# Performance work log

Hardware: AMD Instinct MI355X
Metric: run time of the kernel (lower is better)

## Reference

```python
import jax, jax.numpy as jnp
import numpy as np

B, T, V, E, U, D1, D2, C = 256, 512, 32000, 100, 512, 1024, 1024, 10
SCALE = 0.02


def setup_inputs() -> dict:
    key = jax.random.key(0)
    ks = jax.random.split(key, 12)
    return {
        "tokens": jax.random.randint(ks[0], (B, T), 0, V, dtype=jnp.int32),
        "emb": jax.random.normal(ks[1], (V, E), jnp.float32) * SCALE,
        "Wx": jax.random.normal(ks[2], (E, U), jnp.float32) * SCALE,
        "Wh": jax.random.normal(ks[3], (U, U), jnp.float32) * SCALE,
        "b_rnn": jnp.zeros((U,), jnp.float32),
        "W1": jax.random.normal(ks[4], (U, D1), jnp.float32) * SCALE,
        "b1": jnp.zeros((D1,), jnp.float32),
        "W2": jax.random.normal(ks[5], (D1, D2), jnp.float32) * SCALE,
        "b2": jnp.zeros((D2,), jnp.float32),
        "Wo": jax.random.normal(ks[6], (D2, C), jnp.float32) * SCALE,
        "bo": jnp.zeros((C,), jnp.float32),
    }


def reference(tokens, emb, Wx, Wh, b_rnn, W1, b1, W2, b2, Wo, bo):
    # Embedding with mask_zero=True: token 0 produces a masked timestep.
    x = emb[tokens]                      # [B, T, E]
    mask = tokens != 0                   # [B, T] bool

    # SimpleRNN (activation=relu, return last state). Masked steps carry state.
    xw = jnp.einsum("bte,eu->btu", x, Wx) + b_rnn  # precompute input projection [B,T,U]

    def step(h, inp):
        xw_t, m_t = inp                  # [B,U], [B]
        h_new = jax.nn.relu(xw_t + h @ Wh)
        h = jnp.where(m_t[:, None], h_new, h)
        return h, None

    h0 = jnp.zeros((tokens.shape[0], Wh.shape[0]), x.dtype)
    h_last, _ = jax.lax.scan(step, h0, (jnp.swapaxes(xw, 0, 1), mask.T))

    # MLP head: relu, relu, softmax
    h = jax.nn.relu(h_last @ W1 + b1)
    h = jax.nn.relu(h @ W2 + b2)
    return jax.nn.softmax(h @ Wo + bo, axis=-1)
```

## Files before the change

kernel.cpp:

```cpp
#include <hip/hip_runtime.h>


typedef __attribute__((ext_vector_type(8))) int i32x8_t;
typedef __attribute__((ext_vector_type(4))) float f32x4_t;

constexpr int Bn = 256, Tn = 512, En = 100, Un = 512;
constexpr int D1n = 1024, D2n = 1024, Cn = 10;
constexpr float QS  = 256.f;
constexpr float INV = 1.52587890625e-05f;
constexpr int USC = 0x7F7F7F7F;

__device__ __forceinline__ unsigned f2e4m3_sw(float x) {
    unsigned u = __float_as_uint(x);
    unsigned sgn = (u >> 24) & 0x80;
    float a = __uint_as_float(u & 0x7FFFFFFF);
    if (a >= 448.f) return sgn | 0x7E;
    if (a < 0.015625f) {
        unsigned q = (unsigned)__float2int_rn(a * 512.f);
        return sgn | q;
    }
    int e = (int)((u >> 23) & 0xFF) - 127;
    unsigned m = u & 0x7FFFFF;
    unsigned mant = m >> 20, rem = m & 0xFFFFF;
    if (rem > 0x80000 || (rem == 0x80000 && (mant & 1))) {
        if (++mant == 8) { mant = 0; ++e; }
    }
    if (e > 8) return sgn | 0x7E;
    return sgn | ((unsigned)(e + 7) << 3) | mant;
}

__device__ __forceinline__ unsigned cvt1(float x) {
#if __has_builtin(__builtin_amdgcn_cvt_pk_fp8_f32)
    return (unsigned)__builtin_amdgcn_cvt_pk_fp8_f32(x, x, 0, false) & 0xFFu;
#else
    return f2e4m3_sw(x);
#endif
}

__device__ __forceinline__ unsigned pk4(float a, float b, float c, float d) {
#if __has_builtin(__builtin_amdgcn_cvt_pk_fp8_f32)
    int r = __builtin_amdgcn_cvt_pk_fp8_f32(a, b, 0, false);
    r = __builtin_amdgcn_cvt_pk_fp8_f32(c, d, r, true);
    return (unsigned)r;
#else
    return f2e4m3_sw(a) | (f2e4m3_sw(b) << 8) | (f2e4m3_sw(c) << 16) |
           (f2e4m3_sw(d) << 24);
#endif
}

__global__ __launch_bounds__(256) void pack_wh8(const float* __restrict__ Wh,
                                                unsigned char* __restrict__ P) {
    int e = blockIdx.x * 256 + threadIdx.x;
    int j = e & 31, l = (e >> 5) & 63, kc = (e >> 11) & 3, nt = e >> 13;
    int k = kc * 128 + (l >> 4) * 32 + j;
    int c = nt * 16 + (l & 15);
    P[e] = (unsigned char)cvt1(Wh[k * Un + c] * QS);
}

__global__ __launch_bounds__(256) void pack_wx8(const float* __restrict__ Wx,
                                                unsigned char* __restrict__ P) {
    int e = blockIdx.x * 256 + threadIdx.x;
    int j = e & 31, l = (e >> 5) & 63, nt = e >> 11;
    int k = (l >> 4) * 32 + j;
    int c = nt * 16 + (l & 15);
    P[e] = (k < En) ? (unsigned char)cvt1(Wx[k * Un + c] * QS) : 0;
}

__global__ __launch_bounds__(512, 2) void rnn_persist8(
    const int* __restrict__ tokens, const float* __restrict__ emb,
    const float* __restrict__ b_rnn,
    const unsigned char* __restrict__ WhP8, const unsigned char* __restrict__ WxP8,
    float* __restrict__ h_final)
{
    __shared__ char sh[36864];
    char* H0 = sh;            char* H1 = sh + 8192;
    char* X0 = sh + 16384;    char* X1 = sh + 18432;
    char* TOKB = sh + 20480;

    const int tid  = threadIdx.x;
    const int lane = tid & 63;
    const int wv   = tid >> 6;
    const int r0   = blockIdx.x * 16;

    const int r16  = lane & 15;
    const int q    = lane >> 4;
    const int bswz = r16 << 4;

    for (int f = tid; f < 16 * Tn; f += 512) {
        int row = f >> 9, tt = f & 511;
        *(ushort*)(TOKB + ((((row << 10) | (tt << 1))) ^ (row << 2))) =
            (ushort)tokens[r0 * Tn + f];
    }
    {
        int* z = (int*)sh;
        for (int f = tid; f < 2048; f += 512) z[f] = 0;
        int* zx = (int*)(sh + 16384);
        for (int f = tid; f < 1024; f += 512) zx[f] = 0;
    }
    __syncthreads();

    i32x8_t whf[4][4], wxf[4];
#pragma unroll
    for (int kc = 0; kc < 4; ++kc)
#pragma unroll
        for (int p = 0; p < 4; ++p)
            whf[kc][p] = *(const i32x8_t*)(WhP8 +
                (((wv * 4 + p) * 4 + kc) * 64 + lane) * 32);
#pragma unroll
    for (int p = 0; p < 4; ++p)
        wxf[p] = *(const i32x8_t*)(WxP8 + ((wv * 4 + p) * 64 + lane) * 32);

    float bias_r[4][4];
#pragma unroll
    for (int p = 0; p < 4; ++p)
#pragma unroll
        for (int j = 0; j < 4; ++j)
            bias_r[p][j] = b_rnn[(wv * 4 + p) * 16 + q * 4 + j];

    const int prow = tid / 25;
    const int pc4  = tid - prow * 25;
    const bool is_pref = (tid < 400);
    const int pxaddr = (prow * 128 + pc4 * 4) ^ (prow << 4);

    if (is_pref) {
        int tk = (int)*(const ushort*)(TOKB + (((prow << 10)) ^ (prow << 2)));
        float4 v = *(const float4*)(emb + tk * En + pc4 * 4);
        *(unsigned*)(X0 + pxaddr) = pk4(v.x * QS, v.y * QS, v.z * QS, v.w * QS);
    }
    __syncthreads();

    float hprev[4][4];
#pragma unroll
    for (int p = 0; p < 4; ++p)
#pragma unroll
        for (int j = 0; j < 4; ++j) hprev[p][j] = 0.f;

#define RNN_STEP(T, HC, HN, XC, XN)                                            \
    {                                                                          \
        const int t = (T);                                                     \
        float4 pref;                                                           \
        const bool dp = is_pref && (t + 1 < Tn);                               \
        if (dp) {                                                              \
            int tk = (int)*(const ushort*)(TOKB +                              \
                ((((prow << 10) | ((t + 1) << 1))) ^ (prow << 2)));            \
            pref = *(const float4*)(emb + tk * En + pc4 * 4);                  \
        }                                                                      \
        f32x4_t acc[4];                                                        \
        _Pragma("unroll")                                                      \
        for (int p = 0; p < 4; ++p) acc[p] = (f32x4_t){0.f, 0.f, 0.f, 0.f};    \
        _Pragma("unroll")                                                      \
        for (int kc = 0; kc < 4; ++kc) {                                       \
            const int bb = r16 * 512 + kc * 128 + q * 32;                      \
            uint4 blo = *(const uint4*)((HC) + ((bb) ^ bswz));                 \
            uint4 bhi = *(const uint4*)((HC) + ((bb + 16) ^ bswz));            \
            i32x8_t bf = {(int)blo.x, (int)blo.y, (int)blo.z, (int)blo.w,      \
                          (int)bhi.x, (int)bhi.y, (int)bhi.z, (int)bhi.w};     \
            _Pragma("unroll")                                                  \
            for (int p = 0; p < 4; ++p)                                        \
                acc[p] = __builtin_amdgcn_mfma_scale_f32_16x16x128_f8f6f4(     \
                    whf[kc][p], bf, acc[p], 0, 0, 0, USC, 0, USC);             \
        }                                                                      \
        {                                                                      \
            const int xb = r16 * 128 + q * 32;                                 \
            uint4 blo = *(const uint4*)((XC) + ((xb) ^ bswz));                 \
            uint4 bhi = *(const uint4*)((XC) + ((xb + 16) ^ bswz));            \
            i32x8_t bf = {(int)blo.x, (int)blo.y, (int)blo.z, (int)blo.w,      \
                          (int)bhi.x, (int)bhi.y, (int)bhi.z, (int)bhi.w};     \
            _Pragma("unroll")                                                  \
            for (int p = 0; p < 4; ++p)                                        \
                acc[p] = __builtin_amdgcn_mfma_scale_f32_16x16x128_f8f6f4(     \
                    wxf[p], bf, acc[p], 0, 0, 0, USC, 0, USC);                 \
        }                                                                      \
        const bool mk = *(const ushort*)(TOKB +                                \
            ((((r16 << 10) | (t << 1))) ^ (r16 << 2))) != 0;                   \
        _Pragma("unroll")                                                      \
        for (int p = 0; p < 4; ++p) {                                          \
            float v0 = fmaxf(acc[p][0] * INV + bias_r[p][0], 0.f);             \
            float v1 = fmaxf(acc[p][1] * INV + bias_r[p][1], 0.f);             \
            float v2 = fmaxf(acc[p][2] * INV + bias_r[p][2], 0.f);             \
            float v3 = fmaxf(acc[p][3] * INV + bias_r[p][3], 0.f);             \
            v0 = mk ? v0 : hprev[p][0];  v1 = mk ? v1 : hprev[p][1];           \
            v2 = mk ? v2 : hprev[p][2];  v3 = mk ? v3 : hprev[p][3];           \
            hprev[p][0] = v0; hprev[p][1] = v1;                                \
            hprev[p][2] = v2; hprev[p][3] = v3;                                \
            *(unsigned*)((HN) +                                                \
                ((r16 * 512 + (wv * 4 + p) * 16 + q * 4) ^ bswz)) =            \
                pk4(v0 * QS, v1 * QS, v2 * QS, v3 * QS);                       \
        }                                                                      \
        if (dp) {                                                              \
            *(unsigned*)((XN) + pxaddr) =                                      \
                pk4(pref.x * QS, pref.y * QS, pref.z * QS, pref.w * QS);       \
        }                                                                      \
        __syncthreads();                                                       \
    }

    for (int t2 = 0; t2 < Tn; t2 += 2) {
        RNN_STEP(t2,     H0, H1, X0, X1)
        RNN_STEP(t2 + 1, H1, H0, X1, X0)
    }
#undef RNN_STEP

#pragma unroll
    for (int p = 0; p < 4; ++p) {
        int n = (wv * 4 + p) * 16 + q * 4;
#pragma unroll
        for (int j = 0; j < 4; ++j)
            h_final[(r0 + r16) * Un + n + j] = hprev[p][j];
    }
}

template <int K, bool RELU>
__global__ __launch_bounds__(256) void fc(
    const float* __restrict__ in, const float* __restrict__ W,
    const float* __restrict__ b, float* __restrict__ out, int N)
{
    __shared__ float in_lds[16][K];
    const int tid = threadIdx.x;
    const int r0  = blockIdx.y * 16;
    const int c0  = blockIdx.x * 32;

    for (int i = tid; i < 16 * K; i += 256) {
        int r = i / K, c = i - r * K;
        in_lds[r][c] = in[(r0 + r) * K + c];
    }
    __syncthreads();

    const int col = c0 + (tid & 31);
    const int rb  = (tid >> 5) * 2;

    float acc0 = b[col];
    float acc1 = acc0;
    const float4* i0v = (const float4*)(&in_lds[rb][0]);
    const float4* i1v = (const float4*)(&in_lds[rb + 1][0]);
    for (int k4 = 0; k4 < K / 4; ++k4) {
        float4 a = i0v[k4];
        float4 c = i1v[k4];
        int k = k4 * 4;
        float w0 = W[(k + 0) * N + col];
        float w1 = W[(k + 1) * N + col];
        float w2 = W[(k + 2) * N + col];
        float w3 = W[(k + 3) * N + col];
        acc0 += a.x * w0; acc0 += a.y * w1; acc0 += a.z * w2; acc0 += a.w * w3;
        acc1 += c.x * w0; acc1 += c.y * w1; acc1 += c.z * w2; acc1 += c.w * w3;
    }
    if (RELU) { acc0 = fmaxf(acc0, 0.f); acc1 = fmaxf(acc1, 0.f); }
    out[(r0 + rb) * N + col]     = acc0;
    out[(r0 + rb + 1) * N + col] = acc1;
}

__global__ __launch_bounds__(64) void head_softmax(
    const float* __restrict__ h2, const float* __restrict__ Wo,
    const float* __restrict__ bo, float* __restrict__ out)
{
    const int b    = blockIdx.x;
    const int lane = threadIdx.x;

    float acc[Cn];
#pragma unroll
    for (int c = 0; c < Cn; ++c) acc[c] = 0.f;

    for (int k = lane; k < D2n; k += 64) {
        float hv = h2[b * D2n + k];
#pragma unroll
        for (int c = 0; c < Cn; ++c) acc[c] += hv * Wo[k * Cn + c];
    }
#pragma unroll
    for (int c = 0; c < Cn; ++c) {
#pragma unroll
        for (int off = 32; off > 0; off >>= 1)
            acc[c] += __shfl_down(acc[c], off);
    }
    if (lane == 0) {
        float l[Cn], mx = -1e30f;
#pragma unroll
        for (int c = 0; c < Cn; ++c) { l[c] = acc[c] + bo[c]; mx = fmaxf(mx, l[c]); }
        float s = 0.f;
#pragma unroll
        for (int c = 0; c < Cn; ++c) { l[c] = __expf(l[c] - mx); s += l[c]; }
        float inv = 1.f / s;
#pragma unroll
        for (int c = 0; c < Cn; ++c) out[b * Cn + c] = l[c] * inv;
    }
}

extern "C" void kernel_launch(void* const* d_in, const int* in_sizes, int n_in,
                              void* d_out, int out_size, void* d_ws, size_t ws_size,
                              hipStream_t stream)
{
    const int*   tokens = (const int*)d_in[0];
    const float* emb    = (const float*)d_in[1];
    const float* Wx     = (const float*)d_in[2];
    const float* Wh     = (const float*)d_in[3];
    const float* b_rnn  = (const float*)d_in[4];
    const float* W1     = (const float*)d_in[5];
    const float* b1     = (const float*)d_in[6];
    const float* W2     = (const float*)d_in[7];
    const float* b2     = (const float*)d_in[8];
    const float* Wo     = (const float*)d_in[9];
    const float* bo     = (const float*)d_in[10];
    float* out = (float*)d_out;

    char* ws = (char*)d_ws;
    unsigned char* WhP8 = (unsigned char*)ws;
    unsigned char* WxP8 = (unsigned char*)(ws + (256 << 10));
    float* h_last = (float*)(ws + (320 << 10));
    float* h1     = (float*)(ws + (832 << 10));
    float* h2     = (float*)(ws + (1856 << 10));

    pack_wh8<<<1024, 256, 0, stream>>>(Wh, WhP8);
    pack_wx8<<<256, 256, 0, stream>>>(Wx, WxP8);

    rnn_persist8<<<Bn / 16, 512, 0, stream>>>(
        tokens, emb, b_rnn, WhP8, WxP8, h_last);

    dim3 bs(256);
    fc<Un, true><<<dim3(D1n / 32, Bn / 16), bs, 0, stream>>>(h_last, W1, b1, h1, D1n);
    fc<D1n, true><<<dim3(D2n / 32, Bn / 16), bs, 0, stream>>>(h1, W2, b2, h2, D2n);
    head_softmax<<<Bn, 64, 0, stream>>>(h2, Wo, bo, out);
}
```

Baseline: 586.7 us.

## Precompute input projection in a separate GEMM and prefetch it in the RNN loop

Adds an xw_gemm kernel that gathers embeddings and computes the FP8 input projection plus bias for all timesteps in parallel, storing the result as bf16 in workspace (about 128 MB). The persistent RNN kernel now only prefetches the next step's precomputed projection from global memory instead of gathering embeddings and running an extra MFMA on the serial critical path. The change adds large memory traffic and bf16 rounding of the projection, and it only takes this path when the workspace is large enough. The FC layers also move to 32-row tiles with K chunking, so each weight load is reused across four rows instead of two.

New measurement: 874.6 us. 49.1% more time.

```diff
diff --git a/kernel.cpp b/kernel.cpp
--- a/kernel.cpp
+++ b/kernel.cpp
@@ -48,6 +48,12 @@
 #endif
 }
 
+__device__ __forceinline__ ushort f2bf(float x) {
+    unsigned u = __float_as_uint(x);
+    unsigned r = (u + 0x7FFFu + ((u >> 16) & 1u)) >> 16;
+    return (ushort)r;
+}
+
 __global__ __launch_bounds__(256) void pack_wh8(const float* __restrict__ Wh,
                                                 unsigned char* __restrict__ P) {
     int e = blockIdx.x * 256 + threadIdx.x;
@@ -64,6 +70,193 @@
     int k = (l >> 4) * 32 + j;
     int c = nt * 16 + (l & 15);
     P[e] = (k < En) ? (unsigned char)cvt1(Wx[k * Un + c] * QS) : 0;
+}
+
+__global__ __launch_bounds__(512) void xw_gemm(
+    const int* __restrict__ tokens, const float* __restrict__ emb,
+    const float* __restrict__ b_rnn, const unsigned char* __restrict__ WxP8,
+    ushort* __restrict__ xwp)
+{
+    __shared__ char XS[32768];
+
+    const int tid  = threadIdx.x;
+    const int lane = tid & 63;
+    const int wv   = tid >> 6;
+    const int r0   = blockIdx.x * 16;
+    const int t0   = blockIdx.y * 16;
+
+    const int r16 = lane & 15;
+    const int q   = lane >> 4;
+
+    for (int idx = tid; idx < 6400; idx += 512) {
+        int tt   = idx / 400;
+        int rem  = idx - tt * 400;
+        int prow = rem / 25;
+        int pc4  = rem - prow * 25;
+        int tok  = tokens[(r0 + prow) * Tn + t0 + tt];
+        float4 v = *(const float4*)(emb + tok * En + pc4 * 4);
+        *(unsigned*)(XS + tt * 2048 + ((prow * 128 + pc4 * 4) ^ (prow << 4))) =
+            pk4(v.x * QS, v.y * QS, v.z * QS, v.w * QS);
+    }
+    for (int idx = tid; idx < 16 * 16 * 7; idx += 512) {
+        int tt   = idx / 112;
+        int rem  = idx - tt * 112;
+        int prow = rem / 7;
+        int c4   = 25 + (rem - prow * 7);
+        *(unsigned*)(XS + tt * 2048 + ((prow * 128 + c4 * 4) ^ (prow << 4))) = 0;
+    }
+    __syncthreads();
+
+    i32x8_t wxf[4];
+#pragma unroll
+    for (int p = 0; p < 4; ++p)
+        wxf[p] = *(const i32x8_t*)(WxP8 + ((wv * 4 + p) * 64 + lane) * 32);
+
+    float biasQ[4][4];
+#pragma unroll
+    for (int p = 0; p < 4; ++p)
+#pragma unroll
+        for (int j = 0; j < 4; ++j)
+            biasQ[p][j] = b_rnn[(wv * 4 + p) * 16 + q * 4 + j] * 65536.f;
+
+    const int bswz = r16 << 4;
+    for (int tt = 0; tt < 16; ++tt) {
+        const int xb = tt * 2048 + ((r16 * 128 + q * 32) ^ bswz);
+        uint4 blo = *(const uint4*)(XS + xb);
+        uint4 bhi = *(const uint4*)(XS + (tt * 2048 +
+                        (((r16 * 128 + q * 32) + 16) ^ bswz)));
+        i32x8_t bf = {(int)blo.x, (int)blo.y, (int)blo.z, (int)blo.w,
+                      (int)bhi.x, (int)bhi.y, (int)bhi.z, (int)bhi.w};
+        f32x4_t acc[4];
+#pragma unroll
+        for (int p = 0; p < 4; ++p) {
+            acc[p] = (f32x4_t){biasQ[p][0], biasQ[p][1], biasQ[p][2], biasQ[p][3]};
+            acc[p] = __builtin_amdgcn_mfma_scale_f32_16x16x128_f8f6f4(
+                wxf[p], bf, acc[p], 0, 0, 0, USC, 0, USC);
+        }
+#pragma unroll
+        for (int p = 0; p < 4; ++p) {
+            int n = (wv * 4 + p) * 16 + q * 4;
+            size_t base = ((size_t)(t0 + tt) * Bn + r0 + r16) * Un + n;
+            unsigned u0 = (unsigned)f2bf(acc[p][0]) | ((unsigned)f2bf(acc[p][1]) << 16);
+            unsigned u1 = (unsigned)f2bf(acc[p][2]) | ((unsigned)f2bf(acc[p][3]) << 16);
+            *(uint2*)(xwp + base) = make_uint2(u0, u1);
+        }
+    }
+}
+
+__global__ __launch_bounds__(512, 2) void rnn_persist8x(
+    const int* __restrict__ tokens, const unsigned char* __restrict__ WhP8,
+    const ushort* __restrict__ xwp, float* __restrict__ h_final)
+{
+    __shared__ char sh[32768];
+    char* H0 = sh;            char* H1 = sh + 8192;
+    char* TOKB = sh + 16384;
+
+    const int tid  = threadIdx.x;
+    const int lane = tid & 63;
+    const int wv   = tid >> 6;
+    const int r0   = blockIdx.x * 16;
+
+    const int r16  = lane & 15;
+    const int q    = lane >> 4;
+    const int bswz = r16 << 4;
+
+    for (int f = tid; f < 16 * Tn; f += 512) {
+        int row = f >> 9, tt = f & 511;
+        *(ushort*)(TOKB + ((((row << 10) | (tt << 1))) ^ (row << 2))) =
+            (ushort)tokens[r0 * Tn + f];
+    }
+    {
+        int* z = (int*)sh;
+        for (int f = tid; f < 2048; f += 512) z[f] = 0;
+    }
+    __syncthreads();
+
+    i32x8_t whf[4][4];
+#pragma unroll
+    for (int kc = 0; kc < 4; ++kc)
+#pragma unroll
+        for (int p = 0; p < 4; ++p)
+            whf[kc][p] = *(const i32x8_t*)(WhP8 +
+                (((wv * 4 + p) * 4 + kc) * 64 + lane) * 32);
+
+    const ushort* xwT = xwp + ((size_t)(r0 + r16) * Un + wv * 64 + q * 4);
+
+    float hprev[4][4];
+#pragma unroll
+    for (int p = 0; p < 4; ++p)
+#pragma unroll
+        for (int j = 0; j < 4; ++j) hprev[p][j] = 0.f;
+
+    uint2 pfA[4], pfB[4];
+#pragma unroll
+    for (int p = 0; p < 4; ++p)
+        pfA[p] = *(const uint2*)(xwT + p * 16);
+
+#define BFL(u) __uint_as_float((u) << 16)
+#define BFH(u) __uint_as_float((u) & 0xFFFF0000u)
+
+#define RNN_STEP(T, HC, HN, PFC, PFN)                                          \
+    {                                                                          \
+        const int t = (T);                                                     \
+        if (t + 1 < Tn) {                                                      \
+            const ushort* xt = xwT + (size_t)(t + 1) * (Bn * Un);              \
+            _Pragma("unroll")                                                  \
+            for (int p = 0; p < 4; ++p)                                        \
+                PFN[p] = *(const uint2*)(xt + p * 16);                         \
+        }                                                                      \
+        f32x4_t acc[4];                                                        \
+        _Pragma("unroll")                                                      \
+        for (int p = 0; p < 4; ++p)                                            \
+            acc[p] = (f32x4_t){BFL(PFC[p].x), BFH(PFC[p].x),                   \
+                               BFL(PFC[p].y), BFH(PFC[p].y)};                  \
+        _Pragma("unroll")                                                      \
+        for (int kc = 0; kc < 4; ++kc) {                                       \
+            const int bb = r16 * 512 + kc * 128 + q * 32;                      \
+            uint4 blo = *(const uint4*)((HC) + ((bb) ^ bswz));                 \
+            uint4 bhi = *(const uint4*)((HC) + ((bb + 16) ^ bswz));            \
+            i32x8_t bf = {(int)blo.x, (int)blo.y, (int)blo.z, (int)blo.w,      \
+                          (int)bhi.x, (int)bhi.y, (int)bhi.z, (int)bhi.w};     \
+            _Pragma("unroll")                                                  \
+            for (int p = 0; p < 4; ++p)                                        \
+                acc[p] = __builtin_amdgcn_mfma_scale_f32_16x16x128_f8f6f4(     \
+                    whf[kc][p], bf, acc[p], 0, 0, 0, USC, 0, USC);             \
+        }                                                                      \
+        const bool mk = *(const ushort*)(TOKB +                                \
+            ((((r16 << 10) | (t << 1))) ^ (r16 << 2))) != 0;                   \
+        _Pragma("unroll")                                                      \
+        for (int p = 0; p < 4; ++p) {                                          \
+            float v0 = fmaxf(acc[p][0] * INV, 0.f);                            \
+            float v1 = fmaxf(acc[p][1] * INV, 0.f);                            \
+            float v2 = fmaxf(acc[p][2] * INV, 0.f);                            \
+            float v3 = fmaxf(acc[p][3] * INV, 0.f);                            \
+            v0 = mk ? v0 : hprev[p][0];  v1 = mk ? v1 : hprev[p][1];           \
+            v2 = mk ? v2 : hprev[p][2];  v3 = mk ? v3 : hprev[p][3];           \
+            hprev[p][0] = v0; hprev[p][1] = v1;                                \
+            hprev[p][2] = v2; hprev[p][3] = v3;                                \
+            *(unsigned*)((HN) +                                                \
+                ((r16 * 512 + (wv * 4 + p) * 16 + q * 4) ^ bswz)) =            \
+                pk4(v0 * QS, v1 * QS, v2 * QS, v3 * QS);                       \
+        }                                                                      \
+        __syncthreads();                                                       \
+    }
+
+    for (int t2 = 0; t2 < Tn; t2 += 2) {
+        RNN_STEP(t2,     H0, H1, pfA, pfB)
+        RNN_STEP(t2 + 1, H1, H0, pfB, pfA)
+    }
+#undef RNN_STEP
+#undef BFL
+#undef BFH
+
+#pragma unroll
+    for (int p = 0; p < 4; ++p) {
+        int n = (wv * 4 + p) * 16 + q * 4;
+#pragma unroll
+        for (int j = 0; j < 4; ++j)
+            h_final[(r0 + r16) * Un + n + j] = hprev[p][j];
+    }
 }
 
 __global__ __launch_bounds__(512, 2) void rnn_persist8(
@@ -210,42 +403,53 @@
 }
 
 template <int K, bool RELU>
-__global__ __launch_bounds__(256) void fc(
+__global__ __launch_bounds__(256) void fc32(
     const float* __restrict__ in, const float* __restrict__ W,
     const float* __restrict__ b, float* __restrict__ out, int N)
 {
-    __shared__ float in_lds[16][K];
+    __shared__ float in_lds[32][512];
     const int tid = threadIdx.x;
-    const int r0  = blockIdx.y * 16;
+    const int r0  = blockIdx.y * 32;
     const int c0  = blockIdx.x * 32;
 
-    for (int i = tid; i < 16 * K; i += 256) {
-        int r = i / K, c = i - r * K;
-        in_lds[r][c] = in[(r0 + r) * K + c];
-    }
-    __syncthreads();
-
     const int col = c0 + (tid & 31);
-    const int rb  = (tid >> 5) * 2;
-
-    float acc0 = b[col];
-    float acc1 = acc0;
-    const float4* i0v = (const float4*)(&in_lds[rb][0]);
-    const float4* i1v = (const float4*)(&in_lds[rb + 1][0]);
-    for (int k4 = 0; k4 < K / 4; ++k4) {
-        float4 a = i0v[k4];
-        float4 c = i1v[k4];
-        int k = k4 * 4;
-        float w0 = W[(k + 0) * N + col];
-        float w1 = W[(k + 1) * N + col];
-        float w2 = W[(k + 2) * N + col];
-        float w3 = W[(k + 3) * N + col];
-        acc0 += a.x * w0; acc0 += a.y * w1; acc0 += a.z * w2; acc0 += a.w * w3;
-        acc1 += c.x * w0; acc1 += c.y * w1; acc1 += c.z * w2; acc1 += c.w * w3;
-    }
-    if (RELU) { acc0 = fmaxf(acc0, 0.f); acc1 = fmaxf(acc1, 0.f); }
-    out[(r0 + rb) * N + col]     = acc0;
-    out[(r0 + rb + 1) * N + col] = acc1;
+    const int rq  = (tid >> 5) * 4;
+
+    float acc0 = b[col], acc1 = acc0, acc2 = acc0, acc3 = acc0;
+
+    for (int kc = 0; kc < K / 512; ++kc) {
+        if (kc) __syncthreads();
+        for (int i = tid; i < 32 * 512; i += 256) {
+            int r = i >> 9, c = i & 511;
+            in_lds[r][c] = in[(r0 + r) * K + kc * 512 + c];
+        }
+        __syncthreads();
+
+        const float4* v0 = (const float4*)(&in_lds[rq + 0][0]);
+        const float4* v1 = (const float4*)(&in_lds[rq + 1][0]);
+        const float4* v2 = (const float4*)(&in_lds[rq + 2][0]);
+        const float4* v3 = (const float4*)(&in_lds[rq + 3][0]);
+        for (int k4 = 0; k4 < 128; ++k4) {
+            float4 a0 = v0[k4], a1 = v1[k4], a2 = v2[k4], a3 = v3[k4];
+            int k = kc * 512 + k4 * 4;
+            float w0 = W[(k + 0) * N + col];
+            float w1 = W[(k + 1) * N + col];
+            float w2 = W[(k + 2) * N + col];
+            float w3 = W[(k + 3) * N + col];
+            acc0 += a0.x * w0 + a0.y * w1 + a0.z * w2 + a0.w * w3;
+            acc1 += a1.x * w0 + a1.y * w1 + a1.z * w2 + a1.w * w3;
+            acc2 += a2.x * w0 + a2.y * w1 + a2.z * w2 + a2.w * w3;
+            acc3 += a3.x * w0 + a3.y * w1 + a3.z * w2 + a3.w * w3;
+        }
+    }
+    if (RELU) {
+        acc0 = fmaxf(acc0, 0.f); acc1 = fmaxf(acc1, 0.f);
+        acc2 = fmaxf(acc2, 0.f); acc3 = fmaxf(acc3, 0.f);
+    }
+    out[(r0 + rq + 0) * N + col] = acc0;
+    out[(r0 + rq + 1) * N + col] = acc1;
+    out[(r0 + rq + 2) * N + col] = acc2;
+    out[(r0 + rq + 3) * N + col] = acc3;
 }
 
 __global__ __launch_bounds__(64) void head_softmax(
@@ -306,15 +510,22 @@
     float* h_last = (float*)(ws + (320 << 10));
     float* h1     = (float*)(ws + (832 << 10));
     float* h2     = (float*)(ws + (1856 << 10));
+    ushort* xwp   = (ushort*)(ws + (3u << 20));
+    const size_t need = (3u << 20) + (size_t)Tn * Bn * Un * sizeof(ushort);
 
     pack_wh8<<<1024, 256, 0, stream>>>(Wh, WhP8);
     pack_wx8<<<256, 256, 0, stream>>>(Wx, WxP8);
 
-    rnn_persist8<<<Bn / 16, 512, 0, stream>>>(
-        tokens, emb, b_rnn, WhP8, WxP8, h_last);
+    if (ws_size >= need) {
+        xw_gemm<<<dim3(16, 32), 512, 0, stream>>>(tokens, emb, b_rnn, WxP8, xwp);
+        rnn_persist8x<<<Bn / 16, 512, 0, stream>>>(tokens, WhP8, xwp, h_last);
+    } else {
+        rnn_persist8<<<Bn / 16, 512, 0, stream>>>(
+            tokens, emb, b_rnn, WhP8, WxP8, h_last);
+    }
 
     dim3 bs(256);
-    fc<Un, true><<<dim3(D1n / 32, Bn / 16), bs, 0, stream>>>(h_last, W1, b1, h1, D1n);
-    fc<D1n, true><<<dim3(D2n / 32, Bn / 16), bs, 0, stream>>>(h1, W2, b2, h2, D2n);
+    fc32<Un, true><<<dim3(D1n / 32, Bn / 32), bs, 0, stream>>>(h_last, W1, b1, h1, D1n);
+    fc32<D1n, true><<<dim3(D2n / 32, Bn / 32), bs, 0, stream>>>(h1, W2, b2, h2, D2n);
     head_softmax<<<Bn, 64, 0, stream>>>(h2, Wo, bo, out);
 }
```
